# Kernel optimization log

Hardware: AMD Instinct MI355X
Metric: run time of the kernel (lower is better)

Reference implementation:

```python
import jax, jax.numpy as jnp
import numpy as np

N = 50000
EPS = 1e-16


def _gat_conv(x, w, att_src, att_dst, bias, src, dst, heads, out_ch, concat):
    # x: [N, F_in]; w: [heads*out_ch, F_in]; att_*: [heads, out_ch]; bias: [heads*out_ch] or [out_ch]
    n = x.shape[0]
    xw = (x @ w.T).reshape(n, heads, out_ch)              # [N, H, C]
    a_src = jnp.einsum('nhc,hc->nh', xw, att_src)          # [N, H]
    a_dst = jnp.einsum('nhc,hc->nh', xw, att_dst)
    alpha = a_src[src] + a_dst[dst]                        # [E, H]
    alpha = jax.nn.leaky_relu(alpha, negative_slope=0.2)
    # segment softmax over destination node (every node has a self loop)
    m = jax.ops.segment_max(alpha, dst, num_segments=n)    # [N, H]
    e = jnp.exp(alpha - m[dst])
    s = jax.ops.segment_sum(e, dst, num_segments=n)        # [N, H]
    coef = e / (s[dst] + EPS)                              # [E, H]
    out = jax.ops.segment_sum(xw[src] * coef[:, :, None], dst, num_segments=n)  # [N, H, C]
    if concat:
        out = out.reshape(n, heads * out_ch)
    else:
        out = out.mean(axis=1)
    return out + bias


def setup_inputs() -> dict:
    key = jax.random.key(0)
    ks = jax.random.split(key, 8)
    F_in, H, C1, NC = 128, 2, 64, 16
    E = 1_600_000
    x = jax.random.normal(ks[0], (N, F_in), dtype=jnp.float32)
    edge_index = jax.random.randint(ks[1], (2, E), 0, N, dtype=jnp.int64)
    w1 = jax.random.normal(ks[2], (H * C1, F_in), dtype=jnp.float32) / np.sqrt(F_in)
    att_src1 = jax.random.normal(ks[3], (H, C1), dtype=jnp.float32) / np.sqrt(C1)
    att_dst1 = jax.random.normal(ks[4], (H, C1), dtype=jnp.float32) / np.sqrt(C1)
    b1 = jnp.zeros((H * C1,), dtype=jnp.float32)
    w2 = jax.random.normal(ks[5], (NC, H * C1), dtype=jnp.float32) / np.sqrt(H * C1)
    att_src2 = jax.random.normal(ks[6], (1, NC), dtype=jnp.float32) / np.sqrt(NC)
    att_dst2 = jax.random.normal(ks[7], (1, NC), dtype=jnp.float32) / np.sqrt(NC)
    b2 = jnp.zeros((NC,), dtype=jnp.float32)
    return {"x": x, "edge_index": edge_index, "w1": w1, "att_src1": att_src1,
            "att_dst1": att_dst1, "b1": b1, "w2": w2, "att_src2": att_src2,
            "att_dst2": att_dst2, "b2": b2}


def reference(x, edge_index, w1, att_src1, att_dst1, b1, w2, att_src2, att_dst2, b2):
    n = x.shape[0]
    loop = jnp.arange(n, dtype=edge_index.dtype)
    src = jnp.concatenate([edge_index[0], loop])  # PyG adds self loops by default
    dst = jnp.concatenate([edge_index[1], loop])
    h = _gat_conv(x, w1, att_src1, att_dst1, b1, src, dst, heads=2, out_ch=64, concat=True)
    h = jax.nn.relu(h)
    # dropout p=0.5 is identity in eval mode
    out = _gat_conv(h, w2, att_src2, att_dst2, b2, src, dst, heads=1, out_ch=16, concat=True)
    return out
```

## Files before the change

### kernel.cpp

```cpp
#include <hip/hip_runtime.h>
#include <hip/hip_fp16.h>


#define BSHIFT 7
#define MAXB 512

__device__ __forceinline__ float lrelu(float a) { return fmaxf(a, 0.2f * a); }


__global__ __launch_bounds__(256) void prep_kernel(const float* __restrict__ w1,
                                                   float* __restrict__ w1T,
                                                   int* __restrict__ bincur,
                                                   int B, int CAP) {
  int idx = blockIdx.x * 256 + threadIdx.x;
  int o = idx >> 7, i = idx & 127;
  w1T[i * 128 + o] = w1[idx];
  if (idx < B) bincur[idx] = idx * CAP;
}


__global__ __launch_bounds__(256) void partition_kernel(const int* __restrict__ src,
                                                        const int* __restrict__ dst,
                                                        int* __restrict__ bincur,
                                                        unsigned* __restrict__ binned,
                                                        int E, int B, int CH) {
  __shared__ int s_h[MAXB];
  __shared__ int s_base[MAXB];
  __shared__ int s_cur[MAXB];
  for (int i = threadIdx.x; i < B; i += 256) s_h[i] = 0;
  __syncthreads();
  int lo = blockIdx.x * CH, hi = min(lo + CH, E);
  for (int e = lo + threadIdx.x; e < hi; e += 256)
    atomicAdd(&s_h[dst[e] >> BSHIFT], 1);
  __syncthreads();
  for (int i = threadIdx.x; i < B; i += 256) {
    int c = s_h[i];
    s_base[i] = c ? atomicAdd(&bincur[i], c) : 0;
    s_cur[i] = 0;
  }
  __syncthreads();
  for (int e = lo + threadIdx.x; e < hi; e += 256) {
    int d = dst[e];
    int b = d >> BSHIFT;
    int r = atomicAdd(&s_cur[b], 1);
    binned[s_base[b] + r] = (unsigned)src[e] | ((unsigned)(d & 127) << 16);
  }
}

__global__ __launch_bounds__(256) void bucket_build_kernel(const unsigned* __restrict__ binned,
                                                           const int* __restrict__ bincur,
                                                           int2* __restrict__ nodeseg,
                                                           int* __restrict__ csr,
                                                           int N, int CAP) {
  __shared__ int s_deg[128];
  __shared__ int s_cur[128];
  __shared__ int s_wsum;
  int b = blockIdx.x;
  int lo = b * CAP, hi = bincur[b];
  int t = threadIdx.x;
  if (t < 128) s_deg[t] = 0;
  __syncthreads();
  for (int i = lo + t; i < hi; i += 256)
    atomicAdd(&s_deg[binned[i] >> 16], 1);
  __syncthreads();
  int lane = t & 63, wv = t >> 6;
  int v = (t < 128) ? s_deg[t] : 0;
  int incl = v;
#pragma unroll
  for (int off = 1; off < 64; off <<= 1) {
    int u = __shfl_up(incl, off);
    if (lane >= off) incl += u;
  }
  if (t == 63) s_wsum = incl;
  __syncthreads();
  int excl = incl - v + ((wv == 1) ? s_wsum : 0);
  if (t < 128) {
    int node = (b << BSHIFT) + t;
    if (node < N) nodeseg[node] = make_int2(lo + excl, lo + excl + v);
    s_cur[t] = lo + excl;
  }
  __syncthreads();
  for (int i = lo + t; i < hi; i += 256) {
    unsigned e = binned[i];
    int p = atomicAdd(&s_cur[e >> 16], 1);
    csr[p] = (int)(e & 0xFFFFu);
  }
}


__global__ __launch_bounds__(256) void gemm1_kernel(const float* __restrict__ x,
                                                    const float* __restrict__ w1T,
                                                    const float* __restrict__ as1,
                                                    const float* __restrict__ ad1,
                                                    __half* __restrict__ xw1h,
                                                    float* __restrict__ asrc1,
                                                    float* __restrict__ adst1, int N) {
  __shared__ __align__(16) float xT[128 * 36];
  int t = threadIdx.x;
  int n0 = blockIdx.x * 32;
#pragma unroll
  for (int k = 0; k < 4; ++k) {
    int nd = 8 * k + (t >> 5);
    int i = 4 * (t & 31);
    int gn = n0 + nd;
    float4 v = (gn < N) ? *(const float4*)&x[(size_t)gn * 128 + i]
                        : make_float4(0.f, 0.f, 0.f, 0.f);
    xT[(i + 0) * 36 + nd] = v.x;
    xT[(i + 1) * 36 + nd] = v.y;
    xT[(i + 2) * 36 + nd] = v.z;
    xT[(i + 3) * 36 + nd] = v.w;
  }
  __syncthreads();
  int cg = t & 31, ng = t >> 5;
  int o0 = cg * 4, nlo = ng * 4;
  float acc[4][4];
#pragma unroll
  for (int a = 0; a < 4; ++a)
#pragma unroll
    for (int b = 0; b < 4; ++b) acc[a][b] = 0.f;

#pragma unroll 8
  for (int i = 0; i < 128; ++i) {
    float4 xv = *(const float4*)&xT[i * 36 + nlo];
    float4 wv = *(const float4*)&w1T[i * 128 + o0];
    float xs[4] = {xv.x, xv.y, xv.z, xv.w};
    float ws[4] = {wv.x, wv.y, wv.z, wv.w};
#pragma unroll
    for (int a = 0; a < 4; ++a)
#pragma unroll
      for (int b = 0; b < 4; ++b) acc[a][b] += xs[a] * ws[b];
  }

  float asv[4], adv[4];
#pragma unroll
  for (int b = 0; b < 4; ++b) {
    asv[b] = as1[o0 + b];
    adv[b] = ad1[o0 + b];
  }

#pragma unroll
  for (int a = 0; a < 4; ++a) {
    int n = n0 + nlo + a;
    bool ok = (n < N);
    float ps = 0.f, pd = 0.f;
#pragma unroll
    for (int b = 0; b < 4; ++b) {
      ps += acc[a][b] * asv[b];
      pd += acc[a][b] * adv[b];
    }
#pragma unroll
    for (int k = 1; k < 16; k <<= 1) {
      ps += __shfl_xor(ps, k);
      pd += __shfl_xor(pd, k);
    }
    if (ok && (cg & 15) == 0) {
      int hh = cg >> 4;
      asrc1[2 * n + hh] = ps;
      adst1[2 * n + hh] = pd;
    }
    if (ok) {
      union {
        __half h[4];
        uint2 u;
      } pk;
#pragma unroll
      for (int b = 0; b < 4; ++b) pk.h[b] = __float2half(acc[a][b]);
      *(uint2*)&xw1h[(size_t)n * 128 + o0] = pk.u;
    }
  }
}

__global__ __launch_bounds__(256) void agg1_kernel(const __half* __restrict__ xw1h,
                                                   const float* __restrict__ asrc1,
                                                   const float* __restrict__ adst1,
                                                   const float* __restrict__ b1,
                                                   const float* __restrict__ w2,
                                                   const float* __restrict__ as2,
                                                   const float* __restrict__ ad2,
                                                   const int* __restrict__ csr,
                                                   const int2* __restrict__ nodeseg,
                                                   __half* __restrict__ xw2h,
                                                   float* __restrict__ asrc2,
                                                   float* __restrict__ adst2, int N) {
  __shared__ int s_off[4][64];
  __shared__ float2 s_w[4][64];
  int lane = threadIdx.x & 63, wv = threadIdx.x >> 6;
  int d = blockIdx.x * 4 + wv;
  if (d >= N) return;
  int c8 = lane & 15;
  int row = lane >> 4;
  int head = c8 >> 3;
  int2 seg = nodeseg[d];
  int e0 = seg.x, e1 = seg.y;
  float2 asv = *(const float2*)&asrc1[2 * d];
  float2 adv = *(const float2*)&adst1[2 * d];
  float wself = __expf(lrelu(head ? (asv.y + adv.y) : (asv.x + adv.x)));

  const char* xb = (const char*)xw1h + 16 * c8;

  float a[8];
  float sum = 0.f;
#pragma unroll
  for (int k = 0; k < 8; ++k) a[k] = 0.f;
  if (row == 0) {
    uint4 r = *(const uint4*)(xb + ((size_t)d << 8));
    const __half2* hp = (const __half2*)&r;
#pragma unroll
    for (int k = 0; k < 4; ++k) {
      float2 v = __half22float2(hp[k]);
      a[2 * k] = wself * v.x;
      a[2 * k + 1] = wself * v.y;
    }
    sum = wself;
  }

  for (int base = e0; base < e1; base += 64) {
    int cnt = min(64, e1 - base);
    if (lane < cnt) {
      int s = csr[base + lane];
      float2 aa = *(const float2*)&asrc1[2 * s];
      s_off[wv][lane] = s << 8;
      float2 w;
      w.x = __expf(lrelu(aa.x + adv.x));
      w.y = __expf(lrelu(aa.y + adv.y));
      s_w[wv][lane] = w;
    }
    int j = 0;
    for (; j + 15 < cnt; j += 16) {
      int o0 = s_off[wv][j + row];
      int o1 = s_off[wv][j + 4 + row];
      int o2 = s_off[wv][j + 8 + row];
      int o3 = s_off[wv][j + 12 + row];
      float w0 = ((const float*)&s_w[wv][j + row])[head];
      float w1 = ((const float*)&s_w[wv][j + 4 + row])[head];
      float w2v = ((const float*)&s_w[wv][j + 8 + row])[head];
      float w3 = ((const float*)&s_w[wv][j + 12 + row])[head];
      uint4 r0 = *(const uint4*)(xb + o0);
      uint4 r1 = *(const uint4*)(xb + o1);
      uint4 r2 = *(const uint4*)(xb + o2);
      uint4 r3 = *(const uint4*)(xb + o3);
      const __half2* h0 = (const __half2*)&r0;
      const __half2* h1 = (const __half2*)&r1;
      const __half2* h2 = (const __half2*)&r2;
      const __half2* h3 = (const __half2*)&r3;
#pragma unroll
      for (int k = 0; k < 4; ++k) {
        float2 v0 = __half22float2(h0[k]);
        float2 v1 = __half22float2(h1[k]);
        float2 v2 = __half22float2(h2[k]);
        float2 v3 = __half22float2(h3[k]);
        a[2 * k] += w0 * v0.x + w1 * v1.x + w2v * v2.x + w3 * v3.x;
        a[2 * k + 1] += w0 * v0.y + w1 * v1.y + w2v * v2.y + w3 * v3.y;
      }
      sum += w0 + w1 + w2v + w3;
    }
    for (; j < cnt; j += 4) {
      if (row < cnt - j) {
        int oA = s_off[wv][j + row];
        float wA = ((const float*)&s_w[wv][j + row])[head];
        uint4 rA = *(const uint4*)(xb + oA);
        const __half2* hA = (const __half2*)&rA;
#pragma unroll
        for (int k = 0; k < 4; ++k) {
          float2 vA = __half22float2(hA[k]);
          a[2 * k] += wA * vA.x;
          a[2 * k + 1] += wA * vA.y;
        }
        sum += wA;
      }
    }
  }

#pragma unroll
  for (int k = 0; k < 8; ++k) {
    a[k] += __shfl_xor(a[k], 16);
    a[k] += __shfl_xor(a[k], 32);
  }
  sum += __shfl_xor(sum, 16);
  sum += __shfl_xor(sum, 32);

  float inv = 1.f / (sum + 1e-16f);
  float4 blo = *(const float4*)&b1[8 * c8];
  float4 bhi = *(const float4*)&b1[8 * c8 + 4];
  float h[8];
  h[0] = fmaxf(a[0] * inv + blo.x, 0.f);
  h[1] = fmaxf(a[1] * inv + blo.y, 0.f);
  h[2] = fmaxf(a[2] * inv + blo.z, 0.f);
  h[3] = fmaxf(a[3] * inv + blo.w, 0.f);
  h[4] = fmaxf(a[4] * inv + bhi.x, 0.f);
  h[5] = fmaxf(a[5] * inv + bhi.y, 0.f);
  h[6] = fmaxf(a[6] * inv + bhi.z, 0.f);
  h[7] = fmaxf(a[7] * inv + bhi.w, 0.f);

  float p[4];
#pragma unroll
  for (int cc = 0; cc < 4; ++cc) {
    const float4 wlo = *(const float4*)&w2[(row * 4 + cc) * 128 + 8 * c8];
    const float4 whi = *(const float4*)&w2[(row * 4 + cc) * 128 + 8 * c8 + 4];
    p[cc] = h[0] * wlo.x + h[1] * wlo.y + h[2] * wlo.z + h[3] * wlo.w +
            h[4] * whi.x + h[5] * whi.y + h[6] * whi.z + h[7] * whi.w;
#pragma unroll
    for (int k = 1; k < 16; k <<= 1) p[cc] += __shfl_xor(p[cc], k);
  }
  float qs = 0.f, qd = 0.f;
#pragma unroll
  for (int cc = 0; cc < 4; ++cc) {
    qs += p[cc] * as2[row * 4 + cc];
    qd += p[cc] * ad2[row * 4 + cc];
  }
  qs += __shfl_xor(qs, 16);
  qs += __shfl_xor(qs, 32);
  qd += __shfl_xor(qd, 16);
  qd += __shfl_xor(qd, 32);
  if (lane == 0) {
    asrc2[d] = qs;
    adst2[d] = qd;
  }
  if (c8 == 0) {
    union {
      __half hh[4];
      uint2 u;
    } pk;
#pragma unroll
    for (int cc = 0; cc < 4; ++cc) pk.hh[cc] = __float2half(p[cc]);
    *(uint2*)&xw2h[(size_t)d * 16 + row * 4] = pk.u;
  }
}

__global__ __launch_bounds__(256) void agg2_kernel(const __half* __restrict__ xw2h,
                                                   const float* __restrict__ asrc2,
                                                   const float* __restrict__ adst2,
                                                   const float* __restrict__ b2,
                                                   const int* __restrict__ csr,
                                                   const int2* __restrict__ nodeseg,
                                                   float* __restrict__ out, int N) {
  __shared__ int s_off[4][64];
  __shared__ float s_w[4][64];
  int lane = threadIdx.x & 63, wv = threadIdx.x >> 6;
  int d = blockIdx.x * 4 + wv;
  if (d >= N) return;
  int c2 = lane & 7;
  int row = lane >> 3;
  int2 seg = nodeseg[d];
  int e0 = seg.x, e1 = seg.y;
  float advd = adst2[d];
  float wself = __expf(lrelu(asrc2[d] + advd));
  const char* xb = (const char*)xw2h + 4 * c2;

  float a0 = 0.f, a1 = 0.f, sum = 0.f;
  if (row == 0) {
    float2 v = __half22float2(*(const __half2*)(xb + (size_t)d * 32));
    a0 = wself * v.x;
    a1 = wself * v.y;
    sum = wself;
  }
  for (int base = e0; base < e1; base += 64) {
    int cnt = min(64, e1 - base);
    if (lane < cnt) {
      int s = csr[base + lane];
      s_off[wv][lane] = s << 5;
      s_w[wv][lane] = __expf(lrelu(asrc2[s] + advd));
    }
    int j = 0;
    for (; j + 15 < cnt; j += 16) {
      int o0 = s_off[wv][j + row];
      int o1 = s_off[wv][j + 8 + row];
      float w0 = s_w[wv][j + row];
      float w1 = s_w[wv][j + 8 + row];
      float2 v0 = __half22float2(*(const __half2*)(xb + o0));
      float2 v1 = __half22float2(*(const __half2*)(xb + o1));
      a0 += w0 * v0.x + w1 * v1.x;
      a1 += w0 * v0.y + w1 * v1.y;
      sum += w0 + w1;
    }
    for (; j + 7 < cnt; j += 8) {
      int o0 = s_off[wv][j + row];
      float w0 = s_w[wv][j + row];
      float2 v0 = __half22float2(*(const __half2*)(xb + o0));
      a0 += w0 * v0.x;
      a1 += w0 * v0.y;
      sum += w0;
    }
    if (row < cnt - j) {
      int o0 = s_off[wv][j + row];
      float w0 = s_w[wv][j + row];
      float2 v0 = __half22float2(*(const __half2*)(xb + o0));
      a0 += w0 * v0.x;
      a1 += w0 * v0.y;
      sum += w0;
    }
  }
#pragma unroll
  for (int k = 8; k < 64; k <<= 1) {
    a0 += __shfl_xor(a0, k);
    a1 += __shfl_xor(a1, k);
    sum += __shfl_xor(sum, k);
  }
  if (lane < 8) {
    float inv = 1.f / (sum + 1e-16f);
    float2 r;
    r.x = a0 * inv + b2[2 * c2];
    r.y = a1 * inv + b2[2 * c2 + 1];
    *(float2*)&out[(size_t)d * 16 + 2 * c2] = r;
  }
}


extern "C" void kernel_launch(void* const* d_in, const int* in_sizes, int n_in,
                              void* d_out, int out_size, void* d_ws, size_t ws_size,
                              hipStream_t stream) {
  const float* x = (const float*)d_in[0];
  const int* ei = (const int*)d_in[1];
  const float* w1 = (const float*)d_in[2];
  const float* as1 = (const float*)d_in[3];
  const float* ad1 = (const float*)d_in[4];
  const float* b1 = (const float*)d_in[5];
  const float* w2 = (const float*)d_in[6];
  const float* as2 = (const float*)d_in[7];
  const float* ad2 = (const float*)d_in[8];
  const float* b2 = (const float*)d_in[9];
  float* out = (float*)d_out;

  int N = in_sizes[0] / 128;
  int E = in_sizes[1] / 2;
  const int* srcp = ei;
  const int* dstp = ei + E;

  int B = (N + (1 << BSHIFT) - 1) >> BSHIFT;
  int mean = (E + B - 1) / B;
  int CAP = (mean + mean / 4 + 512 + 255) & ~255;
  const int NB = 256;
  int CH = (E + NB - 1) / NB;

  char* p = (char*)d_ws;
  auto alloc = [&](size_t bytes) -> void* {
    void* r = (void*)p;
    p += (bytes + 255) & ~(size_t)255;
    return r;
  };
  __half* xw1h = (__half*)alloc((size_t)N * 128 * 2);
  float* w1T = (float*)alloc(128 * 128 * 4);
  float* asrc1 = (float*)alloc((size_t)N * 2 * 4);
  float* adst1 = (float*)alloc((size_t)N * 2 * 4);
  __half* xw2h = (__half*)alloc((size_t)N * 16 * 2);
  float* asrc2 = (float*)alloc((size_t)N * 4);
  float* adst2 = (float*)alloc((size_t)N * 4);
  int2* nodeseg = (int2*)alloc((size_t)N * 8);
  int* csr = (int*)alloc((size_t)B * CAP * 4);
  unsigned* binned = (unsigned*)alloc((size_t)B * CAP * 4);
  int* bincur = (int*)alloc((size_t)B * 4);

  prep_kernel<<<64, 256, 0, stream>>>(w1, w1T, bincur, B, CAP);
  partition_kernel<<<NB, 256, 0, stream>>>(srcp, dstp, bincur, binned, E, B, CH);
  bucket_build_kernel<<<B, 256, 0, stream>>>(binned, bincur, nodeseg, csr, N, CAP);

  gemm1_kernel<<<(N + 31) / 32, 256, 0, stream>>>(x, w1T, as1, ad1, xw1h, asrc1, adst1, N);
  agg1_kernel<<<(N + 3) / 4, 256, 0, stream>>>(xw1h, asrc1, adst1, b1, w2, as2, ad2,
                                               csr, nodeseg, xw2h, asrc2, adst2, N);
  agg2_kernel<<<(N + 3) / 4, 256, 0, stream>>>(xw2h, asrc2, adst2, b2, csr, nodeseg, out, N);
}
```

Measured before the change: 249.4 us.

## Use MFMA f16 matrix cores for first-layer GEMM and shrink agg1 unroll

Rewrites gemm1 to convert x and w1 tiles to fp16 in shared memory and compute x@w1^T with 16x16x32 f16 MFMA instructions. Output tiles are staged back through LDS to compute the attention dot products and to write fp16 xw1 rows with wide stores. This removes the separate w1 transpose, which becomes a small cursor-init kernel. The agg1 inner loop drops from 4 to 2 gathered rows per iteration, which lowers register pressure. The GEMM inputs now lose precision to fp16 before the multiply, and the attention logits are computed from fp16-rounded outputs.

```diff
diff --git a/kernel.cpp b/kernel.cpp
--- a/kernel.cpp
+++ b/kernel.cpp
@@ -5,19 +5,18 @@
 #define BSHIFT 7
 #define MAXB 512
 
+using f16x8 = __attribute__((ext_vector_type(8))) _Float16;
+using f16x4 = __attribute__((ext_vector_type(4))) _Float16;
+using f32x4 = __attribute__((ext_vector_type(4))) float;
+
 __device__ __forceinline__ float lrelu(float a) { return fmaxf(a, 0.2f * a); }
 
 
-__global__ __launch_bounds__(256) void prep_kernel(const float* __restrict__ w1,
-                                                   float* __restrict__ w1T,
-                                                   int* __restrict__ bincur,
-                                                   int B, int CAP) {
-  int idx = blockIdx.x * 256 + threadIdx.x;
-  int o = idx >> 7, i = idx & 127;
-  w1T[i * 128 + o] = w1[idx];
-  if (idx < B) bincur[idx] = idx * CAP;
-}
-
+__global__ __launch_bounds__(256) void init_cursor_kernel(int* __restrict__ bincur,
+                                                          int B, int CAP) {
+  int i = blockIdx.x * 256 + threadIdx.x;
+  if (i < B) bincur[i] = i * CAP;
+}
 
 __global__ __launch_bounds__(256) void partition_kernel(const int* __restrict__ src,
                                                         const int* __restrict__ dst,
@@ -88,84 +87,102 @@
 }
 
 
+#define XS 136
 __global__ __launch_bounds__(256) void gemm1_kernel(const float* __restrict__ x,
-                                                    const float* __restrict__ w1T,
+                                                    const float* __restrict__ w1,
                                                     const float* __restrict__ as1,
                                                     const float* __restrict__ ad1,
                                                     __half* __restrict__ xw1h,
                                                     float* __restrict__ asrc1,
                                                     float* __restrict__ adst1, int N) {
-  __shared__ __align__(16) float xT[128 * 36];
+  __shared__ __align__(16) _Float16 lx[64 * XS];
+  __shared__ __align__(16) _Float16 lw[128 * XS];
   int t = threadIdx.x;
-  int n0 = blockIdx.x * 32;
-#pragma unroll
-  for (int k = 0; k < 4; ++k) {
-    int nd = 8 * k + (t >> 5);
-    int i = 4 * (t & 31);
+  int n0 = blockIdx.x * 64;
+
+#pragma unroll
+  for (int j = 0; j < 8; ++j) {
+    int idx = t + 256 * j;
+    int nd = idx >> 5, i4 = (idx & 31) * 4;
     int gn = n0 + nd;
-    float4 v = (gn < N) ? *(const float4*)&x[(size_t)gn * 128 + i]
+    float4 v = (gn < N) ? *(const float4*)&x[(size_t)gn * 128 + i4]
                         : make_float4(0.f, 0.f, 0.f, 0.f);
-    xT[(i + 0) * 36 + nd] = v.x;
-    xT[(i + 1) * 36 + nd] = v.y;
-    xT[(i + 2) * 36 + nd] = v.z;
-    xT[(i + 3) * 36 + nd] = v.w;
-  }
-  __syncthreads();
-  int cg = t & 31, ng = t >> 5;
-  int o0 = cg * 4, nlo = ng * 4;
-  float acc[4][4];
-#pragma unroll
-  for (int a = 0; a < 4; ++a)
-#pragma unroll
-    for (int b = 0; b < 4; ++b) acc[a][b] = 0.f;
-
-#pragma unroll 8
-  for (int i = 0; i < 128; ++i) {
-    float4 xv = *(const float4*)&xT[i * 36 + nlo];
-    float4 wv = *(const float4*)&w1T[i * 128 + o0];
-    float xs[4] = {xv.x, xv.y, xv.z, xv.w};
-    float ws[4] = {wv.x, wv.y, wv.z, wv.w};
-#pragma unroll
-    for (int a = 0; a < 4; ++a)
-#pragma unroll
-      for (int b = 0; b < 4; ++b) acc[a][b] += xs[a] * ws[b];
-  }
-
-  float asv[4], adv[4];
-#pragma unroll
-  for (int b = 0; b < 4; ++b) {
-    asv[b] = as1[o0 + b];
-    adv[b] = ad1[o0 + b];
-  }
-
-#pragma unroll
-  for (int a = 0; a < 4; ++a) {
-    int n = n0 + nlo + a;
-    bool ok = (n < N);
+    f16x4 h;
+    h[0] = (_Float16)v.x; h[1] = (_Float16)v.y;
+    h[2] = (_Float16)v.z; h[3] = (_Float16)v.w;
+    *(f16x4*)&lx[nd * XS + i4] = h;
+  }
+#pragma unroll
+  for (int j = 0; j < 16; ++j) {
+    int idx = t + 256 * j;
+    int o = idx >> 5, i4 = (idx & 31) * 4;
+    float4 v = *(const float4*)&w1[(size_t)o * 128 + i4];
+    f16x4 h;
+    h[0] = (_Float16)v.x; h[1] = (_Float16)v.y;
+    h[2] = (_Float16)v.z; h[3] = (_Float16)v.w;
+    *(f16x4*)&lw[o * XS + i4] = h;
+  }
+  __syncthreads();
+
+  int lane = t & 63, wv = t >> 6;
+  int m16 = lane & 15, q = lane >> 4;
+
+  f32x4 acc[8];
+#pragma unroll
+  for (int i = 0; i < 8; ++i) acc[i] = (f32x4){0.f, 0.f, 0.f, 0.f};
+
+#pragma unroll
+  for (int c = 0; c < 4; ++c) {
+    f16x8 a = *(const f16x8*)&lx[(16 * wv + m16) * XS + c * 32 + q * 8];
+#pragma unroll
+    for (int tt = 0; tt < 8; ++tt) {
+      f16x8 b = *(const f16x8*)&lw[(tt * 16 + m16) * XS + c * 32 + q * 8];
+      acc[tt] = __builtin_amdgcn_mfma_f32_16x16x32_f16(a, b, acc[tt], 0, 0, 0);
+    }
+  }
+
+#pragma unroll
+  for (int tt = 0; tt < 8; ++tt) {
+#pragma unroll
+    for (int r = 0; r < 4; ++r) {
+      lx[(16 * wv + 4 * q + r) * XS + tt * 16 + m16] = (_Float16)acc[tt][r];
+    }
+  }
+
+  {
     float ps = 0.f, pd = 0.f;
-#pragma unroll
-    for (int b = 0; b < 4; ++b) {
-      ps += acc[a][b] * asv[b];
-      pd += acc[a][b] * adv[b];
-    }
-#pragma unroll
-    for (int k = 1; k < 16; k <<= 1) {
-      ps += __shfl_xor(ps, k);
-      pd += __shfl_xor(pd, k);
-    }
-    if (ok && (cg & 15) == 0) {
-      int hh = cg >> 4;
+    int p = q;
+#pragma unroll
+    for (int k = 0; k < 4; ++k) {
+      f16x8 hv = *(const f16x8*)&lx[(16 * wv + m16) * XS + p * 32 + k * 8];
+      float4 s0 = *(const float4*)&as1[p * 32 + k * 8];
+      float4 s1 = *(const float4*)&as1[p * 32 + k * 8 + 4];
+      float4 d0 = *(const float4*)&ad1[p * 32 + k * 8];
+      float4 d1 = *(const float4*)&ad1[p * 32 + k * 8 + 4];
+      ps += (float)hv[0] * s0.x + (float)hv[1] * s0.y + (float)hv[2] * s0.z +
+            (float)hv[3] * s0.w + (float)hv[4] * s1.x + (float)hv[5] * s1.y +
+            (float)hv[6] * s1.z + (float)hv[7] * s1.w;
+      pd += (float)hv[0] * d0.x + (float)hv[1] * d0.y + (float)hv[2] * d0.z +
+            (float)hv[3] * d0.w + (float)hv[4] * d1.x + (float)hv[5] * d1.y +
+            (float)hv[6] * d1.z + (float)hv[7] * d1.w;
+    }
+    ps += __shfl_xor(ps, 16);
+    pd += __shfl_xor(pd, 16);
+    int n = n0 + 16 * wv + m16;
+    if (n < N && (q == 0 || q == 2)) {
+      int hh = q >> 1;
       asrc1[2 * n + hh] = ps;
       adst1[2 * n + hh] = pd;
     }
-    if (ok) {
-      union {
-        __half h[4];
-        uint2 u;
-      } pk;
-#pragma unroll
-      for (int b = 0; b < 4; ++b) pk.h[b] = __float2half(acc[a][b]);
-      *(uint2*)&xw1h[(size_t)n * 128 + o0] = pk.u;
+  }
+
+#pragma unroll
+  for (int i = 0; i < 4; ++i) {
+    int m = q + 4 * i;
+    int n = n0 + 16 * wv + m;
+    if (n < N) {
+      uint4 v = *(const uint4*)&lx[(16 * wv + m) * XS + m16 * 8];
+      *(uint4*)&xw1h[(size_t)n * 128 + m16 * 8] = v;
     }
   }
 }
@@ -226,33 +243,23 @@
       s_w[wv][lane] = w;
     }
     int j = 0;
-    for (; j + 15 < cnt; j += 16) {
-      int o0 = s_off[wv][j + row];
-      int o1 = s_off[wv][j + 4 + row];
-      int o2 = s_off[wv][j + 8 + row];
-      int o3 = s_off[wv][j + 12 + row];
-      float w0 = ((const float*)&s_w[wv][j + row])[head];
-      float w1 = ((const float*)&s_w[wv][j + 4 + row])[head];
-      float w2v = ((const float*)&s_w[wv][j + 8 + row])[head];
-      float w3 = ((const float*)&s_w[wv][j + 12 + row])[head];
-      uint4 r0 = *(const uint4*)(xb + o0);
-      uint4 r1 = *(const uint4*)(xb + o1);
-      uint4 r2 = *(const uint4*)(xb + o2);
-      uint4 r3 = *(const uint4*)(xb + o3);
-      const __half2* h0 = (const __half2*)&r0;
-      const __half2* h1 = (const __half2*)&r1;
-      const __half2* h2 = (const __half2*)&r2;
-      const __half2* h3 = (const __half2*)&r3;
+    for (; j + 7 < cnt; j += 8) {
+      int oA = s_off[wv][j + row];
+      int oB = s_off[wv][j + 4 + row];
+      float wA = ((const float*)&s_w[wv][j + row])[head];
+      float wB = ((const float*)&s_w[wv][j + 4 + row])[head];
+      uint4 rA = *(const uint4*)(xb + oA);
+      uint4 rB = *(const uint4*)(xb + oB);
+      const __half2* hA = (const __half2*)&rA;
+      const __half2* hB = (const __half2*)&rB;
 #pragma unroll
       for (int k = 0; k < 4; ++k) {
-        float2 v0 = __half22float2(h0[k]);
-        float2 v1 = __half22float2(h1[k]);
-        float2 v2 = __half22float2(h2[k]);
-        float2 v3 = __half22float2(h3[k]);
-        a[2 * k] += w0 * v0.x + w1 * v1.x + w2v * v2.x + w3 * v3.x;
-        a[2 * k + 1] += w0 * v0.y + w1 * v1.y + w2v * v2.y + w3 * v3.y;
+        float2 vA = __half22float2(hA[k]);
+        float2 vB = __half22float2(hB[k]);
+        a[2 * k] += wA * vA.x + wB * vB.x;
+        a[2 * k + 1] += wA * vA.y + wB * vB.y;
       }
-      sum += w0 + w1 + w2v + w3;
+      sum += wA + wB;
     }
     for (; j < cnt; j += 4) {
       if (row < cnt - j) {
@@ -439,7 +446,6 @@
     return r;
   };
   __half* xw1h = (__half*)alloc((size_t)N * 128 * 2);
-  float* w1T = (float*)alloc(128 * 128 * 4);
   float* asrc1 = (float*)alloc((size_t)N * 2 * 4);
   float* adst1 = (float*)alloc((size_t)N * 2 * 4);
   __half* xw2h = (__half*)alloc((size_t)N * 16 * 2);
@@ -450,11 +456,11 @@
   unsigned* binned = (unsigned*)alloc((size_t)B * CAP * 4);
   int* bincur = (int*)alloc((size_t)B * 4);
 
-  prep_kernel<<<64, 256, 0, stream>>>(w1, w1T, bincur, B, CAP);
+  init_cursor_kernel<<<(B + 255) / 256, 256, 0, stream>>>(bincur, B, CAP);
   partition_kernel<<<NB, 256, 0, stream>>>(srcp, dstp, bincur, binned, E, B, CH);
   bucket_build_kernel<<<B, 256, 0, stream>>>(binned, bincur, nodeseg, csr, N, CAP);
 
-  gemm1_kernel<<<(N + 31) / 32, 256, 0, stream>>>(x, w1T, as1, ad1, xw1h, asrc1, adst1, N);
+  gemm1_kernel<<<(N + 63) / 64, 256, 0, stream>>>(x, w1, as1, ad1, xw1h, asrc1, adst1, N);
   agg1_kernel<<<(N + 3) / 4, 256, 0, stream>>>(xw1h, asrc1, adst1, b1, w2, as2, ad2,
                                                csr, nodeseg, xw2h, asrc2, adst2, N);
   agg2_kernel<<<(N + 3) / 4, 256, 0, stream>>>(xw2h, asrc2, adst2, b2, csr, nodeseg, out, N);
```

New measurement: 227.4 us. -8.8%, faster.
